# Performance work log

Hardware: AMD Instinct MI355X
Metric: run time of the kernel (lower is better)

Reference implementation:

```python
import jax, jax.numpy as jnp
import numpy as np


def _kernelize(data, projection_matrix):
    # FAVOR+ positive softmax features: ratio * h(x) * f(x @ P^T)
    # h(x) = exp(-||x||^2 / 2), f(u) = exp(u)
    d = data.shape[-1]
    r = projection_matrix.shape[0]
    data_norm = (d ** -0.25) * data                       # [n, d]
    ratio = r ** -0.5
    data_dash = jnp.einsum('id,rd->ir', data_norm, projection_matrix)  # [n, r]
    h = jnp.exp(-0.5 * jnp.sum(data_norm * data_norm, axis=-1, keepdims=True))  # [n, 1]
    return ratio * h * jnp.exp(data_dash)                 # [n, r]


def setup_inputs() -> dict:
    key = jax.random.key(0)
    k1, k2, k3, k4 = jax.random.split(key, 4)
    n, d, dv, r = 65536, 64, 64, 256
    q = jax.random.normal(k1, (n, d), dtype=jnp.float32)
    k = jax.random.normal(k2, (n, d), dtype=jnp.float32)
    v = jax.random.normal(k3, (n, dv), dtype=jnp.float32)
    projection_matrix = jax.random.normal(k4, (r, d), dtype=jnp.float32)
    return {"q": q, "k": k, "v": v, "projection_matrix": projection_matrix}


def reference(q, k, v, projection_matrix):
    q_hat = _kernelize(q, projection_matrix)              # [n, r]
    k_hat = _kernelize(k, projection_matrix)              # [n, r]
    z = k_hat.T @ v                                       # [r, dv]  (FAVOR associativity)
    w = q_hat @ z                                         # [n, dv]
    d_inv = 1.0 / jnp.sum(q_hat * jnp.sum(k_hat, axis=0), axis=1, keepdims=True)  # [n, 1]
    return d_inv * w
```

## Files before the change

kernel.cpp:

```cpp
#include <hip/hip_runtime.h>
#include <math.h>

typedef __attribute__((ext_vector_type(8))) short bf16x8;
typedef __attribute__((ext_vector_type(4))) float f32x4;

#define NROWS 65536
#define RFEAT 256
#define DDIM 64
#define NCOL 80
#define PARTN (RFEAT * NCOL)
#define NGROUP 16

#define SCLOG2E 0.51006971688f
#define RC_COEF -0.09016844006f
#define LOG2RATIO -4.0f

__device__ __forceinline__ unsigned short f2bf(float f) {
    union { float f; unsigned int u; } v; v.f = f;
    unsigned int r = v.u + 0x7FFFu + ((v.u >> 16) & 1u);
    return (unsigned short)(r >> 16);
}

__global__ __launch_bounds__(256)
void prep_kernel(const float* __restrict__ P, const float* __restrict__ V,
                 unsigned short* __restrict__ Pb, unsigned short* __restrict__ Vb)
{
    const int t = threadIdx.x, l = t & 63;
    if (blockIdx.x == 2048) {
        const int g = t >> 6;
        for (int f = g * 8; f < g * 8 + 8; f++) {
            const int kstep = f >> 4, nt = f & 15;
            const float* src = P + (nt * 16 + (l & 15)) * 64 + kstep * 32 + (l >> 4) * 8;
            bf16x8 frag;
            #pragma unroll
            for (int j = 0; j < 8; j++) frag[j] = (short)f2bf(SCLOG2E * src[j]);
            *(bf16x8*)(Pb + f * 512 + l * 8) = frag;
        }
        return;
    }
    const int F = blockIdx.x * 4 + (t >> 6);
    const float* src = V + (size_t)((F >> 2) * 32 + (l >> 4) * 8) * 64 + (F & 3) * 16 + (l & 15);
    bf16x8 fr;
    #pragma unroll
    for (int j = 0; j < 8; j++) fr[j] = (short)f2bf(src[j * 64]);
    *(bf16x8*)(Vb + (size_t)F * 512 + l * 8) = fr;
}

template<int LDP, bool TRANS>
__device__ __forceinline__ void phi_chunk(const float* __restrict__ X, int chunkBase,
                                          const unsigned short* __restrict__ Pb,
                                          unsigned short* phi_lds, float* rc)
{
    const int t = threadIdx.x, l = t & 63, w = t >> 6;
    if (t < 64) {
        const float4* xr = (const float4*)(X + (size_t)(chunkBase + t) * 64);
        float s0 = 0.f, s1 = 0.f;
        #pragma unroll
        for (int j = 0; j < 16; j += 2) {
            float4 a = xr[j];     s0 += a.x*a.x + a.y*a.y + a.z*a.z + a.w*a.w;
            float4 b = xr[j + 1]; s1 += b.x*b.x + b.y*b.y + b.z*b.z + b.w*b.w;
        }
        rc[t] = RC_COEF * (s0 + s1) + LOG2RATIO;
    }
    const float* ar = X + (size_t)(chunkBase + 16 * w + (l & 15)) * 64 + (l >> 4) * 8;
    bf16x8 a0, a1;
    #pragma unroll
    for (int j = 0; j < 8; j++) a0[j] = (short)f2bf(ar[j]);
    #pragma unroll
    for (int j = 0; j < 8; j++) a1[j] = (short)f2bf(ar[32 + j]);
    __syncthreads();
    const float4 rcv = *(const float4*)(rc + 16 * w + 4 * (l >> 4));
    #pragma unroll
    for (int nt = 0; nt < 16; nt++) {
        bf16x8 b0 = *(const bf16x8*)(Pb + nt * 512 + l * 8);
        bf16x8 b1 = *(const bf16x8*)(Pb + (16 + nt) * 512 + l * 8);
        f32x4 acc = (f32x4){rcv.x, rcv.y, rcv.z, rcv.w};
        acc = __builtin_amdgcn_mfma_f32_16x16x32_bf16(a0, b0, acc, 0, 0, 0);
        acc = __builtin_amdgcn_mfma_f32_16x16x32_bf16(a1, b1, acc, 0, 0, 0);
        float p0 = __builtin_amdgcn_exp2f(acc[0]);
        float p1 = __builtin_amdgcn_exp2f(acc[1]);
        float p2 = __builtin_amdgcn_exp2f(acc[2]);
        float p3 = __builtin_amdgcn_exp2f(acc[3]);
        const int col = nt * 16 + (l & 15);
        unsigned int w0 = (unsigned int)f2bf(p0) | ((unsigned int)f2bf(p1) << 16);
        unsigned int w1 = (unsigned int)f2bf(p2) | ((unsigned int)f2bf(p3) << 16);
        if (TRANS) {
            unsigned int* dst = (unsigned int*)(phi_lds + col * LDP + 16 * w + 4 * (l >> 4));
            dst[0] = w0;
            dst[1] = w1;
        } else {
            const int rb = (16 * w + (l >> 4) * 4) * LDP + col;
            phi_lds[rb]           = (unsigned short)(w0);
            phi_lds[rb + LDP]     = (unsigned short)(w0 >> 16);
            phi_lds[rb + 2 * LDP] = (unsigned short)(w1);
            phi_lds[rb + 3 * LDP] = (unsigned short)(w1 >> 16);
        }
    }
    __syncthreads();
}

__global__ __launch_bounds__(256, 2)
void kv_fused_kernel(const float* __restrict__ Kp, const unsigned short* __restrict__ Vb,
                     const unsigned short* __restrict__ Pb,
                     float* __restrict__ partials, int chunksPerBlock)
{
    __shared__ __align__(16) unsigned short phi_lds[RFEAT * 72];
    __shared__ __align__(16) float rc[64];
    const int t = threadIdx.x, l = t & 63, w = t >> 6;

    f32x4 acc[4][5];
    #pragma unroll
    for (int mt = 0; mt < 4; mt++)
        #pragma unroll
        for (int nt = 0; nt < 5; nt++) acc[mt][nt] = (f32x4){0.f, 0.f, 0.f, 0.f};

    bf16x8 ones;
    #pragma unroll
    for (int j = 0; j < 8; j++) ones[j] = (short)(((l & 15) == 0) ? 0x3F80 : 0);

    const int base = blockIdx.x * chunksPerBlock * 64;
    for (int c = 0; c < chunksPerBlock; c++) {
        const int cb = base + c * 64;
        phi_chunk<72, true>(Kp, cb, Pb, phi_lds, rc);
        #pragma unroll
        for (int ks = 0; ks < 2; ks++) {
            bf16x8 af[4];
            #pragma unroll
            for (int mt = 0; mt < 4; mt++)
                af[mt] = *(const bf16x8*)(phi_lds + (64 * w + mt * 16 + (l & 15)) * 72
                                          + ks * 32 + (l >> 4) * 8);
            const unsigned short* vb = Vb + ((size_t)((cb >> 5) + ks) * 4) * 512 + l * 8;
            bf16x8 bf4[4];
            #pragma unroll
            for (int nt = 0; nt < 4; nt++) bf4[nt] = *(const bf16x8*)(vb + nt * 512);
            #pragma unroll
            for (int mt = 0; mt < 4; mt++) {
                #pragma unroll
                for (int nt = 0; nt < 4; nt++)
                    acc[mt][nt] = __builtin_amdgcn_mfma_f32_16x16x32_bf16(af[mt], bf4[nt], acc[mt][nt], 0, 0, 0);
                acc[mt][4] = __builtin_amdgcn_mfma_f32_16x16x32_bf16(af[mt], ones, acc[mt][4], 0, 0, 0);
            }
        }
    }
    float* slot = partials + (size_t)blockIdx.x * PARTN;
    #pragma unroll
    for (int mt = 0; mt < 4; mt++)
        #pragma unroll
        for (int nt = 0; nt < 5; nt++)
            #pragma unroll
            for (int reg = 0; reg < 4; reg++)
                slot[(64 * w + mt * 16 + (l >> 4) * 4 + reg) * 80 + nt * 16 + (l & 15)] = acc[mt][nt][reg];
}

__global__ __launch_bounds__(256)
void reduce1_kernel(const float* __restrict__ partials, float* __restrict__ p2,
                    int slotsPerGroup)
{
    const int idx = blockIdx.x * 256 + threadIdx.x;
    const int g = blockIdx.y;
    const float* base = partials + (size_t)g * slotsPerGroup * PARTN + idx;
    float s0 = 0.f, s1 = 0.f, s2 = 0.f, s3 = 0.f;
    int b = 0;
    for (; b + 4 <= slotsPerGroup; b += 4) {
        s0 += base[(size_t)(b + 0) * PARTN];
        s1 += base[(size_t)(b + 1) * PARTN];
        s2 += base[(size_t)(b + 2) * PARTN];
        s3 += base[(size_t)(b + 3) * PARTN];
    }
    for (; b < slotsPerGroup; b++) s0 += base[(size_t)b * PARTN];
    p2[(size_t)g * PARTN + idx] = (s0 + s1) + (s2 + s3);
}

__global__ __launch_bounds__(256)
void reduce2_kernel(const float* __restrict__ p2, unsigned short* __restrict__ Zb, int ngroups)
{
    const int idx = blockIdx.x * 256 + threadIdx.x;
    float s = 0.f;
    for (int g = 0; g < ngroups; g++) s += p2[(size_t)g * PARTN + idx];
    const int m = idx / 80, n = idx - m * 80;
    Zb[((m >> 3) * 80 + n) * 8 + (m & 7)] = f2bf(s);
}

__global__ __launch_bounds__(256, 2)
void q_out_kernel(const float* __restrict__ Q, const unsigned short* __restrict__ Pb,
                  const unsigned short* __restrict__ Zb, float* __restrict__ out)
{
    __shared__ __align__(16) unsigned short phi_lds[64 * 272];
    __shared__ __align__(16) float rc[64];
    const int t = threadIdx.x, l = t & 63, w = t >> 6;
    const int base = blockIdx.x * 64;

    phi_chunk<272, false>(Q, base, Pb, phi_lds, rc);

    f32x4 acc[5];
    #pragma unroll
    for (int nt = 0; nt < 5; nt++) acc[nt] = (f32x4){0.f, 0.f, 0.f, 0.f};

    #pragma unroll
    for (int ks = 0; ks < 8; ks++) {
        bf16x8 a = *(const bf16x8*)(phi_lds + (16 * w + (l & 15)) * 272 + ks * 32 + (l >> 4) * 8);
        #pragma unroll
        for (int nt = 0; nt < 5; nt++) {
            bf16x8 b = *(const bf16x8*)(Zb + ((ks * 4 + (l >> 4)) * 80 + nt * 16 + (l & 15)) * 8);
            acc[nt] = __builtin_amdgcn_mfma_f32_16x16x32_bf16(a, b, acc[nt], 0, 0, 0);
        }
    }
    float inv[4];
    #pragma unroll
    for (int reg = 0; reg < 4; reg++) {
        float den = __shfl(acc[4][reg], (l & 48));
        inv[reg] = 1.0f / den;
    }
    const int row = base + 16 * w + (l >> 4) * 4;
    #pragma unroll
    for (int nt = 0; nt < 4; nt++)
        #pragma unroll
        for (int reg = 0; reg < 4; reg++)
            out[(size_t)(row + reg) * 64 + nt * 16 + (l & 15)] = acc[nt][reg] * inv[reg];
}

extern "C" void kernel_launch(void* const* d_in, const int* in_sizes, int n_in,
                              void* d_out, int out_size, void* d_ws, size_t ws_size,
                              hipStream_t stream) {
    const float* q = (const float*)d_in[0];
    const float* k = (const float*)d_in[1];
    const float* v = (const float*)d_in[2];
    const float* P = (const float*)d_in[3];
    float* out = (float*)d_out;

    unsigned short* Pb = (unsigned short*)d_ws;
    unsigned short* Zb = Pb + 32 * 512;
    unsigned short* Vb = (unsigned short*)((char*)d_ws + 73728);
    float* p2 = (float*)((char*)d_ws + 73728 + 8388608);
    float* partials = p2 + (size_t)NGROUP * PARTN;

    long fixedBytes = 73728 + 8388608 + (long)NGROUP * PARTN * 4;
    long avail = ((long)ws_size - fixedBytes) / (long)(PARTN * 4);
    int NB = 512;
    while (NB > NGROUP && (long)NB > avail) NB >>= 1;
    int chunks = 1024 / NB;
    int ngroups = (NB >= NGROUP) ? NGROUP : NB;
    int spg = NB / ngroups;

    prep_kernel<<<2049, 256, 0, stream>>>(P, v, Pb, Vb);
    kv_fused_kernel<<<NB, 256, 0, stream>>>(k, Vb, Pb, partials, chunks);
    reduce1_kernel<<<dim3(80, ngroups), 256, 0, stream>>>(partials, p2, spg);
    reduce2_kernel<<<80, 256, 0, stream>>>(p2, Zb, ngroups);
    q_out_kernel<<<1024, 256, 0, stream>>>(q, Pb, Zb, out);
}
```

Measured before the change: 139.4 us.

## Replace partial-sum reduction kernels with float atomics into Z

```diff
diff --git a/kernel.cpp b/kernel.cpp
--- a/kernel.cpp
+++ b/kernel.cpp
@@ -4,12 +4,9 @@
 typedef __attribute__((ext_vector_type(8))) short bf16x8;
 typedef __attribute__((ext_vector_type(4))) float f32x4;
 
-#define NROWS 65536
 #define RFEAT 256
-#define DDIM 64
-#define NCOL 80
-#define PARTN (RFEAT * NCOL)
-#define NGROUP 16
+#define ZN 20480
+#define NBKV 256
 
 #define SCLOG2E 0.51006971688f
 #define RC_COEF -0.09016844006f
@@ -23,9 +20,19 @@
 
 __global__ __launch_bounds__(256)
 void prep_kernel(const float* __restrict__ P, const float* __restrict__ V,
-                 unsigned short* __restrict__ Pb, unsigned short* __restrict__ Vb)
+                 unsigned short* __restrict__ Pb, unsigned short* __restrict__ Vb,
+                 float* __restrict__ Zf)
 {
     const int t = threadIdx.x, l = t & 63;
+    if (blockIdx.x < 2048) {
+        const int F = blockIdx.x * 4 + (t >> 6);
+        const float* src = V + (size_t)((F >> 2) * 32 + (l >> 4) * 8) * 64 + (F & 3) * 16 + (l & 15);
+        bf16x8 fr;
+        #pragma unroll
+        for (int j = 0; j < 8; j++) fr[j] = (short)f2bf(src[j * 64]);
+        *(bf16x8*)(Vb + (size_t)F * 512 + l * 8) = fr;
+        return;
+    }
     if (blockIdx.x == 2048) {
         const int g = t >> 6;
         for (int f = g * 8; f < g * 8 + 8; f++) {
@@ -38,12 +45,8 @@
         }
         return;
     }
-    const int F = blockIdx.x * 4 + (t >> 6);
-    const float* src = V + (size_t)((F >> 2) * 32 + (l >> 4) * 8) * 64 + (F & 3) * 16 + (l & 15);
-    bf16x8 fr;
-    #pragma unroll
-    for (int j = 0; j < 8; j++) fr[j] = (short)f2bf(src[j * 64]);
-    *(bf16x8*)(Vb + (size_t)F * 512 + l * 8) = fr;
+    const int idx = (blockIdx.x - 2049) * 256 + t;
+    Zf[idx] = 0.f;
 }
 
 template<int LDP, bool TRANS>
@@ -100,9 +103,8 @@
 }
 
 __global__ __launch_bounds__(256, 2)
-void kv_fused_kernel(const float* __restrict__ Kp, const unsigned short* __restrict__ Vb,
-                     const unsigned short* __restrict__ Pb,
-                     float* __restrict__ partials, int chunksPerBlock)
+void kv_atomic_kernel(const float* __restrict__ Kp, const unsigned short* __restrict__ Vb,
+                      const unsigned short* __restrict__ Pb, float* __restrict__ Zf)
 {
     __shared__ __align__(16) unsigned short phi_lds[RFEAT * 72];
     __shared__ __align__(16) float rc[64];
@@ -118,8 +120,8 @@
     #pragma unroll
     for (int j = 0; j < 8; j++) ones[j] = (short)(((l & 15) == 0) ? 0x3F80 : 0);
 
-    const int base = blockIdx.x * chunksPerBlock * 64;
-    for (int c = 0; c < chunksPerBlock; c++) {
+    const int base = blockIdx.x * 256;
+    for (int c = 0; c < 4; c++) {
         const int cb = base + c * 64;
         phi_chunk<72, true>(Kp, cb, Pb, phi_lds, rc);
         #pragma unroll
@@ -142,54 +144,35 @@
             }
         }
     }
-    float* slot = partials + (size_t)blockIdx.x * PARTN;
-    #pragma unroll
-    for (int mt = 0; mt < 4; mt++)
-        #pragma unroll
-        for (int nt = 0; nt < 5; nt++)
+    #pragma unroll
+    for (int mt = 0; mt < 4; mt++) {
+        #pragma unroll
+        for (int nt = 0; nt < 5; nt++) {
+            if (nt == 4 && (l & 15) != 0) continue;
             #pragma unroll
             for (int reg = 0; reg < 4; reg++)
-                slot[(64 * w + mt * 16 + (l >> 4) * 4 + reg) * 80 + nt * 16 + (l & 15)] = acc[mt][nt][reg];
-}
-
-__global__ __launch_bounds__(256)
-void reduce1_kernel(const float* __restrict__ partials, float* __restrict__ p2,
-                    int slotsPerGroup)
-{
-    const int idx = blockIdx.x * 256 + threadIdx.x;
-    const int g = blockIdx.y;
-    const float* base = partials + (size_t)g * slotsPerGroup * PARTN + idx;
-    float s0 = 0.f, s1 = 0.f, s2 = 0.f, s3 = 0.f;
-    int b = 0;
-    for (; b + 4 <= slotsPerGroup; b += 4) {
-        s0 += base[(size_t)(b + 0) * PARTN];
-        s1 += base[(size_t)(b + 1) * PARTN];
-        s2 += base[(size_t)(b + 2) * PARTN];
-        s3 += base[(size_t)(b + 3) * PARTN];
-    }
-    for (; b < slotsPerGroup; b++) s0 += base[(size_t)b * PARTN];
-    p2[(size_t)g * PARTN + idx] = (s0 + s1) + (s2 + s3);
-}
-
-__global__ __launch_bounds__(256)
-void reduce2_kernel(const float* __restrict__ p2, unsigned short* __restrict__ Zb, int ngroups)
-{
-    const int idx = blockIdx.x * 256 + threadIdx.x;
-    float s = 0.f;
-    for (int g = 0; g < ngroups; g++) s += p2[(size_t)g * PARTN + idx];
-    const int m = idx / 80, n = idx - m * 80;
-    Zb[((m >> 3) * 80 + n) * 8 + (m & 7)] = f2bf(s);
+                unsafeAtomicAdd(&Zf[(64 * w + mt * 16 + (l >> 4) * 4 + reg) * 80
+                                    + nt * 16 + (l & 15)], acc[mt][nt][reg]);
+        }
+    }
 }
 
 __global__ __launch_bounds__(256, 2)
 void q_out_kernel(const float* __restrict__ Q, const unsigned short* __restrict__ Pb,
-                  const unsigned short* __restrict__ Zb, float* __restrict__ out)
+                  const float* __restrict__ Zf, float* __restrict__ out)
 {
     __shared__ __align__(16) unsigned short phi_lds[64 * 272];
+    __shared__ __align__(16) unsigned short zb_lds[ZN];
     __shared__ __align__(16) float rc[64];
     const int t = threadIdx.x, l = t & 63, w = t >> 6;
     const int base = blockIdx.x * 64;
 
+    #pragma unroll 4
+    for (int i = 0; i < 80; i++) {
+        const int idx = i * 256 + t;
+        const int m = idx / 80, n = idx - m * 80;
+        zb_lds[((m >> 3) * 80 + n) * 8 + (m & 7)] = f2bf(Zf[idx]);
+    }
     phi_chunk<272, false>(Q, base, Pb, phi_lds, rc);
 
     f32x4 acc[5];
@@ -201,7 +184,7 @@
         bf16x8 a = *(const bf16x8*)(phi_lds + (16 * w + (l & 15)) * 272 + ks * 32 + (l >> 4) * 8);
         #pragma unroll
         for (int nt = 0; nt < 5; nt++) {
-            bf16x8 b = *(const bf16x8*)(Zb + ((ks * 4 + (l >> 4)) * 80 + nt * 16 + (l & 15)) * 8);
+            bf16x8 b = *(const bf16x8*)(zb_lds + ((ks * 4 + (l >> 4)) * 80 + nt * 16 + (l & 15)) * 8);
             acc[nt] = __builtin_amdgcn_mfma_f32_16x16x32_bf16(a, b, acc[nt], 0, 0, 0);
         }
     }
@@ -229,22 +212,10 @@
     float* out = (float*)d_out;
 
     unsigned short* Pb = (unsigned short*)d_ws;
-    unsigned short* Zb = Pb + 32 * 512;
-    unsigned short* Vb = (unsigned short*)((char*)d_ws + 73728);
-    float* p2 = (float*)((char*)d_ws + 73728 + 8388608);
-    float* partials = p2 + (size_t)NGROUP * PARTN;
-
-    long fixedBytes = 73728 + 8388608 + (long)NGROUP * PARTN * 4;
-    long avail = ((long)ws_size - fixedBytes) / (long)(PARTN * 4);
-    int NB = 512;
-    while (NB > NGROUP && (long)NB > avail) NB >>= 1;
-    int chunks = 1024 / NB;
-    int ngroups = (NB >= NGROUP) ? NGROUP : NB;
-    int spg = NB / ngroups;
-
-    prep_kernel<<<2049, 256, 0, stream>>>(P, v, Pb, Vb);
-    kv_fused_kernel<<<NB, 256, 0, stream>>>(k, Vb, Pb, partials, chunks);
-    reduce1_kernel<<<dim3(80, ngroups), 256, 0, stream>>>(partials, p2, spg);
-    reduce2_kernel<<<80, 256, 0, stream>>>(p2, Zb, ngroups);
-    q_out_kernel<<<1024, 256, 0, stream>>>(q, Pb, Zb, out);
-}
+    float* Zf = (float*)((char*)d_ws + 32768);
+    unsigned short* Vb = (unsigned short*)((char*)d_ws + 32768 + 81920);
+
+    prep_kernel<<<2129, 256, 0, stream>>>(P, v, Pb, Vb, Zf);
+    kv_atomic_kernel<<<NBKV, 256, 0, stream>>>(k, Vb, Pb, Zf);
+    q_out_kernel<<<1024, 256, 0, stream>>>(q, Pb, Zf, out);
+}
```

New measurement: 154.8 us. 1.11x slower.

## Widen KV kernel to 512-thread blocks processing one 128-row chunk each

Applied to the files above, without the earlier changes.

```diff
diff --git a/kernel.cpp b/kernel.cpp
--- a/kernel.cpp
+++ b/kernel.cpp
@@ -4,12 +4,12 @@
 typedef __attribute__((ext_vector_type(8))) short bf16x8;
 typedef __attribute__((ext_vector_type(4))) float f32x4;
 
-#define NROWS 65536
 #define RFEAT 256
-#define DDIM 64
 #define NCOL 80
 #define PARTN (RFEAT * NCOL)
+#define NBKV 512
 #define NGROUP 16
+#define LDK 136
 
 #define SCLOG2E 0.51006971688f
 #define RC_COEF -0.09016844006f
@@ -26,33 +26,32 @@
                  unsigned short* __restrict__ Pb, unsigned short* __restrict__ Vb)
 {
     const int t = threadIdx.x, l = t & 63;
-    if (blockIdx.x == 2048) {
-        const int g = t >> 6;
-        for (int f = g * 8; f < g * 8 + 8; f++) {
-            const int kstep = f >> 4, nt = f & 15;
-            const float* src = P + (nt * 16 + (l & 15)) * 64 + kstep * 32 + (l >> 4) * 8;
-            bf16x8 frag;
-            #pragma unroll
-            for (int j = 0; j < 8; j++) frag[j] = (short)f2bf(SCLOG2E * src[j]);
-            *(bf16x8*)(Pb + f * 512 + l * 8) = frag;
-        }
+    if (blockIdx.x < 2048) {
+        const int F = blockIdx.x * 4 + (t >> 6);
+        const float* src = V + (size_t)((F >> 2) * 32 + (l >> 4) * 8) * 64 + (F & 3) * 16 + (l & 15);
+        bf16x8 fr;
+        #pragma unroll
+        for (int j = 0; j < 8; j++) fr[j] = (short)f2bf(src[j * 64]);
+        *(bf16x8*)(Vb + (size_t)F * 512 + l * 8) = fr;
         return;
     }
-    const int F = blockIdx.x * 4 + (t >> 6);
-    const float* src = V + (size_t)((F >> 2) * 32 + (l >> 4) * 8) * 64 + (F & 3) * 16 + (l & 15);
-    bf16x8 fr;
-    #pragma unroll
-    for (int j = 0; j < 8; j++) fr[j] = (short)f2bf(src[j * 64]);
-    *(bf16x8*)(Vb + (size_t)F * 512 + l * 8) = fr;
-}
-
-template<int LDP, bool TRANS>
-__device__ __forceinline__ void phi_chunk(const float* __restrict__ X, int chunkBase,
-                                          const unsigned short* __restrict__ Pb,
-                                          unsigned short* phi_lds, float* rc)
-{
-    const int t = threadIdx.x, l = t & 63, w = t >> 6;
-    if (t < 64) {
+    const int g = t >> 6;
+    for (int f = g * 8; f < g * 8 + 8; f++) {
+        const int kstep = f >> 4, nt = f & 15;
+        const float* src = P + (nt * 16 + (l & 15)) * 64 + kstep * 32 + (l >> 4) * 8;
+        bf16x8 frag;
+        #pragma unroll
+        for (int j = 0; j < 8; j++) frag[j] = (short)f2bf(SCLOG2E * src[j]);
+        *(bf16x8*)(Pb + f * 512 + l * 8) = frag;
+    }
+}
+
+__device__ __forceinline__ void phi_chunk8(const float* __restrict__ X, int chunkBase,
+                                           const unsigned short* __restrict__ Pb,
+                                           unsigned short* phi_lds, float* rc)
+{
+    const int t = threadIdx.x, l = t & 63, w = t >> 6;
+    if (t < 128) {
         const float4* xr = (const float4*)(X + (size_t)(chunkBase + t) * 64);
         float s0 = 0.f, s1 = 0.f;
         #pragma unroll
@@ -84,33 +83,24 @@
         const int col = nt * 16 + (l & 15);
         unsigned int w0 = (unsigned int)f2bf(p0) | ((unsigned int)f2bf(p1) << 16);
         unsigned int w1 = (unsigned int)f2bf(p2) | ((unsigned int)f2bf(p3) << 16);
-        if (TRANS) {
-            unsigned int* dst = (unsigned int*)(phi_lds + col * LDP + 16 * w + 4 * (l >> 4));
-            dst[0] = w0;
-            dst[1] = w1;
-        } else {
-            const int rb = (16 * w + (l >> 4) * 4) * LDP + col;
-            phi_lds[rb]           = (unsigned short)(w0);
-            phi_lds[rb + LDP]     = (unsigned short)(w0 >> 16);
-            phi_lds[rb + 2 * LDP] = (unsigned short)(w1);
-            phi_lds[rb + 3 * LDP] = (unsigned short)(w1 >> 16);
-        }
-    }
-    __syncthreads();
-}
-
-__global__ __launch_bounds__(256, 2)
-void kv_fused_kernel(const float* __restrict__ Kp, const unsigned short* __restrict__ Vb,
-                     const unsigned short* __restrict__ Pb,
-                     float* __restrict__ partials, int chunksPerBlock)
-{
-    __shared__ __align__(16) unsigned short phi_lds[RFEAT * 72];
-    __shared__ __align__(16) float rc[64];
-    const int t = threadIdx.x, l = t & 63, w = t >> 6;
-
-    f32x4 acc[4][5];
-    #pragma unroll
-    for (int mt = 0; mt < 4; mt++)
+        unsigned int* dst = (unsigned int*)(phi_lds + col * LDK + 16 * w + 4 * (l >> 4));
+        dst[0] = w0;
+        dst[1] = w1;
+    }
+    __syncthreads();
+}
+
+__global__ __launch_bounds__(512, 4)
+void kv_kernel(const float* __restrict__ Kp, const unsigned short* __restrict__ Vb,
+               const unsigned short* __restrict__ Pb, float* __restrict__ partials)
+{
+    __shared__ __align__(16) unsigned short phi_lds[RFEAT * LDK];
+    __shared__ __align__(16) float rc[128];
+    const int t = threadIdx.x, l = t & 63, w = t >> 6;
+
+    f32x4 acc[2][5];
+    #pragma unroll
+    for (int mt = 0; mt < 2; mt++)
         #pragma unroll
         for (int nt = 0; nt < 5; nt++) acc[mt][nt] = (f32x4){0.f, 0.f, 0.f, 0.f};
 
@@ -118,38 +108,36 @@
     #pragma unroll
     for (int j = 0; j < 8; j++) ones[j] = (short)(((l & 15) == 0) ? 0x3F80 : 0);
 
-    const int base = blockIdx.x * chunksPerBlock * 64;
-    for (int c = 0; c < chunksPerBlock; c++) {
-        const int cb = base + c * 64;
-        phi_chunk<72, true>(Kp, cb, Pb, phi_lds, rc);
-        #pragma unroll
-        for (int ks = 0; ks < 2; ks++) {
-            bf16x8 af[4];
+    const int cb = blockIdx.x * 128;
+    phi_chunk8(Kp, cb, Pb, phi_lds, rc);
+
+    #pragma unroll
+    for (int ks = 0; ks < 4; ks++) {
+        bf16x8 af[2];
+        #pragma unroll
+        for (int mt = 0; mt < 2; mt++)
+            af[mt] = *(const bf16x8*)(phi_lds + (32 * w + mt * 16 + (l & 15)) * LDK
+                                      + ks * 32 + (l >> 4) * 8);
+        const unsigned short* vb = Vb + ((size_t)((cb >> 5) + ks) * 4) * 512 + l * 8;
+        bf16x8 bf4[4];
+        #pragma unroll
+        for (int nt = 0; nt < 4; nt++) bf4[nt] = *(const bf16x8*)(vb + nt * 512);
+        #pragma unroll
+        for (int mt = 0; mt < 2; mt++) {
             #pragma unroll
-            for (int mt = 0; mt < 4; mt++)
-                af[mt] = *(const bf16x8*)(phi_lds + (64 * w + mt * 16 + (l & 15)) * 72
-                                          + ks * 32 + (l >> 4) * 8);
-            const unsigned short* vb = Vb + ((size_t)((cb >> 5) + ks) * 4) * 512 + l * 8;
-            bf16x8 bf4[4];
-            #pragma unroll
-            for (int nt = 0; nt < 4; nt++) bf4[nt] = *(const bf16x8*)(vb + nt * 512);
-            #pragma unroll
-            for (int mt = 0; mt < 4; mt++) {
-                #pragma unroll
-                for (int nt = 0; nt < 4; nt++)
-                    acc[mt][nt] = __builtin_amdgcn_mfma_f32_16x16x32_bf16(af[mt], bf4[nt], acc[mt][nt], 0, 0, 0);
-                acc[mt][4] = __builtin_amdgcn_mfma_f32_16x16x32_bf16(af[mt], ones, acc[mt][4], 0, 0, 0);
-            }
+            for (int nt = 0; nt < 4; nt++)
+                acc[mt][nt] = __builtin_amdgcn_mfma_f32_16x16x32_bf16(af[mt], bf4[nt], acc[mt][nt], 0, 0, 0);
+            acc[mt][4] = __builtin_amdgcn_mfma_f32_16x16x32_bf16(af[mt], ones, acc[mt][4], 0, 0, 0);
         }
     }
     float* slot = partials + (size_t)blockIdx.x * PARTN;
     #pragma unroll
-    for (int mt = 0; mt < 4; mt++)
+    for (int mt = 0; mt < 2; mt++)
         #pragma unroll
         for (int nt = 0; nt < 5; nt++)
             #pragma unroll
             for (int reg = 0; reg < 4; reg++)
-                slot[(64 * w + mt * 16 + (l >> 4) * 4 + reg) * 80 + nt * 16 + (l & 15)] = acc[mt][nt][reg];
+                slot[(32 * w + mt * 16 + (l >> 4) * 4 + reg) * 80 + nt * 16 + (l & 15)] = acc[mt][nt][reg];
 }
 
 __global__ __launch_bounds__(256)
@@ -181,7 +169,53 @@
     Zb[((m >> 3) * 80 + n) * 8 + (m & 7)] = f2bf(s);
 }
 
-__global__ __launch_bounds__(256, 2)
+__device__ __forceinline__ void phi_chunk_q(const float* __restrict__ X, int chunkBase,
+                                            const unsigned short* __restrict__ Pb,
+                                            unsigned short* phi_lds, float* rc)
+{
+    const int t = threadIdx.x, l = t & 63, w = t >> 6;
+    if (t < 64) {
+        const float4* xr = (const float4*)(X + (size_t)(chunkBase + t) * 64);
+        float s0 = 0.f, s1 = 0.f;
+        #pragma unroll
+        for (int j = 0; j < 16; j += 2) {
+            float4 a = xr[j];     s0 += a.x*a.x + a.y*a.y + a.z*a.z + a.w*a.w;
+            float4 b = xr[j + 1]; s1 += b.x*b.x + b.y*b.y + b.z*b.z + b.w*b.w;
+        }
+        rc[t] = RC_COEF * (s0 + s1) + LOG2RATIO;
+    }
+    const float* ar = X + (size_t)(chunkBase + 16 * w + (l & 15)) * 64 + (l >> 4) * 8;
+    bf16x8 a0, a1;
+    #pragma unroll
+    for (int j = 0; j < 8; j++) a0[j] = (short)f2bf(ar[j]);
+    #pragma unroll
+    for (int j = 0; j < 8; j++) a1[j] = (short)f2bf(ar[32 + j]);
+    __syncthreads();
+    const float4 rcv = *(const float4*)(rc + 16 * w + 4 * (l >> 4));
+    #pragma unroll
+    for (int nt = 0; nt < 16; nt++) {
+        bf16x8 b0 = *(const bf16x8*)(Pb + nt * 512 + l * 8);
+        bf16x8 b1 = *(const bf16x8*)(Pb + (16 + nt) * 512 + l * 8);
+        f32x4 acc = (f32x4){rcv.x, rcv.y, rcv.z, rcv.w};
+        acc = __builtin_amdgcn_mfma_f32_16x16x32_bf16(a0, b0, acc, 0, 0, 0);
+        acc = __builtin_amdgcn_mfma_f32_16x16x32_bf16(a1, b1, acc, 0, 0, 0);
+        float p0 = __builtin_amdgcn_exp2f(acc[0]);
+        float p1 = __builtin_amdgcn_exp2f(acc[1]);
+        float p2 = __builtin_amdgcn_exp2f(acc[2]);
+        float p3 = __builtin_amdgcn_exp2f(acc[3]);
+        const int col = nt * 16 + (l & 15);
+        unsigned int w0 = (unsigned int)f2bf(p0) | ((unsigned int)f2bf(p1) << 16);
+        unsigned int w1 = (unsigned int)f2bf(p2) | ((unsigned int)f2bf(p3) << 16);
+        const int rb = (16 * w + (l >> 4) * 4) * 272 + col;
+        phi_lds[rb]         = (unsigned short)(w0);
+        phi_lds[rb + 272]   = (unsigned short)(w0 >> 16);
+        phi_lds[rb + 544]   = (unsigned short)(w1);
+        phi_lds[rb + 816]   = (unsigned short)(w1 >> 16);
+    }
+    __syncthreads();
+}
+
+__global__ __launch_bounds__(256, 4)
 void q_out_kernel(const float* __restrict__ Q, const unsigned short* __restrict__ Pb,
                   const unsigned short* __restrict__ Zb, float* __restrict__ out)
 {
@@ -190,7 +224,7 @@
     const int t = threadIdx.x, l = t & 63, w = t >> 6;
     const int base = blockIdx.x * 64;
 
-    phi_chunk<272, false>(Q, base, Pb, phi_lds, rc);
+    phi_chunk_q(Q, base, Pb, phi_lds, rc);
 
     f32x4 acc[5];
     #pragma unroll
@@ -234,17 +268,9 @@
     float* p2 = (float*)((char*)d_ws + 73728 + 8388608);
     float* partials = p2 + (size_t)NGROUP * PARTN;
 
-    long fixedBytes = 73728 + 8388608 + (long)NGROUP * PARTN * 4;
-    long avail = ((long)ws_size - fixedBytes) / (long)(PARTN * 4);
-    int NB = 512;
-    while (NB > NGROUP && (long)NB > avail) NB >>= 1;
-    int chunks = 1024 / NB;
-    int ngroups = (NB >= NGROUP) ? NGROUP : NB;
-    int spg = NB / ngroups;
-
     prep_kernel<<<2049, 256, 0, stream>>>(P, v, Pb, Vb);
-    kv_fused_kernel<<<NB, 256, 0, stream>>>(k, Vb, Pb, partials, chunks);
-    reduce1_kernel<<<dim3(80, ngroups), 256, 0, stream>>>(partials, p2, spg);
-    reduce2_kernel<<<80, 256, 0, stream>>>(p2, Zb, ngroups);
+    kv_kernel<<<NBKV, 512, 0, stream>>>(k, Vb, Pb, partials);
+    reduce1_kernel<<<dim3(80, NGROUP), 256, 0, stream>>>(partials, p2, 32);
+    reduce2_kernel<<<80, 256, 0, stream>>>(p2, Zb, NGROUP);
     q_out_kernel<<<1024, 256, 0, stream>>>(q, Pb, Zb, out);
 }
```

After: 138.0 us. Within noise of the previous version (-1.0%).
